# Performance work log

Hardware: AMD Instinct MI355X
Metric: run time of the kernel (lower is better)

## Reference

```python
import jax, jax.numpy as jnp
import numpy as np

N_NODES = 100000
D_FEAT = 128
UNITS = 128
N_EDGES = 600000


def setup_inputs() -> dict:
    key = jax.random.key(0)
    k1, k2, k3, k4, k5 = jax.random.split(key, 5)
    X = jax.random.normal(k1, (N_NODES, D_FEAT), dtype=jnp.float32)
    ref_a = jax.random.randint(k2, (N_EDGES,), 0, N_NODES, dtype=jnp.int32)
    ref_b = jax.random.randint(k3, (N_EDGES,), 0, N_NODES, dtype=jnp.int32)
    # Glorot-ish scaled dense weights
    W_hidden = jax.random.normal(k4, (D_FEAT, UNITS), dtype=jnp.float32) * (1.0 / np.sqrt(D_FEAT))
    W_out = jax.random.normal(k5, (UNITS, UNITS), dtype=jnp.float32) * (1.0 / np.sqrt(UNITS))
    b_hidden = jnp.zeros((UNITS,), dtype=jnp.float32)
    b_out = jnp.zeros((UNITS,), dtype=jnp.float32)
    return dict(X=X, ref_a=ref_a, ref_b=ref_b, W_hidden=W_hidden,
                b_hidden=b_hidden, W_out=W_out, b_out=b_out)


def wl1_convolution(X, ref_a, ref_b):
    # WL1 neighborhood aggregation over undirected edges (ref_a, ref_b):
    # each node keeps its own features plus the sum of its neighbors'.
    n = X.shape[0]
    agg_a = jax.ops.segment_sum(X[ref_b], ref_a, num_segments=n)  # [N, D]
    agg_b = jax.ops.segment_sum(X[ref_a], ref_b, num_segments=n)  # [N, D]
    return X + agg_a + agg_b


def reference(X, ref_a, ref_b, W_hidden, b_hidden, W_out, b_out):
    X_agg = wl1_convolution(X, ref_a, ref_b)                 # [N, D]
    X_hid = jax.nn.relu(X_agg @ W_hidden + b_hidden)          # [N, U] (inner_activation=relu)
    X_out = X_hid @ W_out + b_out                             # [N, U] (activation=linear)
    return X_out
```

## Files before the change

### kernel.cpp

```cpp
#include <hip/hip_runtime.h>

#define CAP 64

typedef short bf16x8 __attribute__((ext_vector_type(8)));
typedef float f32x4 __attribute__((ext_vector_type(4)));
typedef unsigned short u16;
typedef unsigned int u32;

__device__ __forceinline__ u16 f32_to_bf16(float f) {
  u32 b = __float_as_uint(f);
  b += 0x7fffu + ((b >> 16) & 1u);
  return (u16)(b >> 16);
}

__global__ void convert_x_kernel(const float* __restrict__ X,
                                 u16* __restrict__ Xb, int n8) {
  int i = blockIdx.x * blockDim.x + threadIdx.x;
  if (i >= n8) return;
  float4 a = ((const float4*)X)[2 * i];
  float4 b = ((const float4*)X)[2 * i + 1];
  int4 o;
  o.x = (int)((u32)f32_to_bf16(a.x) | ((u32)f32_to_bf16(a.y) << 16));
  o.y = (int)((u32)f32_to_bf16(a.z) | ((u32)f32_to_bf16(a.w) << 16));
  o.z = (int)((u32)f32_to_bf16(b.x) | ((u32)f32_to_bf16(b.y) << 16));
  o.w = (int)((u32)f32_to_bf16(b.z) | ((u32)f32_to_bf16(b.w) << 16));
  ((int4*)Xb)[i] = o;
}

__global__ __launch_bounds__(256) void fill_adj_xcd_kernel(
    const int* __restrict__ ra, const int* __restrict__ rb,
    int* __restrict__ cnt, int* __restrict__ adj, int nedges) {
  const int myx = blockIdx.x & 7;
  const int slice = blockIdx.x >> 3;
  int t = slice * 256 + threadIdx.x;
  int e0 = t * 2;
  if (e0 >= nedges) return;
  bool has1 = (e0 + 1) < nedges;
  int2 av = ((const int2*)ra)[t];
  int2 bv = ((const int2*)rb)[t];

  int d[4], s[4];
  d[0] = av.x; s[0] = bv.x;
  d[1] = bv.x; s[1] = av.x;
  d[2] = has1 ? av.y : -1; s[2] = bv.y;
  d[3] = has1 ? bv.y : -1; s[3] = av.y;
#pragma unroll
  for (int i = 0; i < 4; ++i) {
    if (d[i] >= 0 && (d[i] & 7) == myx) {
      int p = atomicAdd(&cnt[d[i]], 1);
      if (p < CAP) adj[(size_t)d[i] * CAP + p] = s[i];
    }
  }
}

__global__ void gather_agg_kernel(const u16* __restrict__ Xb,
                                  const int* __restrict__ cnt,
                                  int* __restrict__ adj,
                                  int nnodes) {
  int gid = blockIdx.x * blockDim.x + threadIdx.x;
  int wid = gid >> 6;
  int l = gid & 63;
  int half = l >> 5;
  int hl = l & 31;
  int node = wid * 2 + half;
  if (node >= nnodes) return;
  const uint2* Xv = (const uint2*)Xb;
  const int* lst = adj + (size_t)node * CAP;
  int idx0 = lst[hl];
  int idx1 = lst[hl + 32];
  int n = cnt[node];
  if (n > CAP) n = CAP;
  uint2 ps = Xv[(size_t)node * 32 + hl];
  float a0 = __uint_as_float(ps.x << 16);
  float a1 = __uint_as_float(ps.x & 0xffff0000u);
  float a2 = __uint_as_float(ps.y << 16);
  float a3 = __uint_as_float(ps.y & 0xffff0000u);
  const int base = half << 5;
  for (int k = 0; k < n; k += 8) {
    uint2 pv[8];
#pragma unroll
    for (int t = 0; t < 8; ++t) {
      int pos = k + t;
      int sel = (pos < 32) ? idx0 : idx1;
      int nb = __shfl(sel, base + (pos & 31));
      pv[t] = (pos < n) ? Xv[(size_t)nb * 32 + hl] : make_uint2(0u, 0u);
    }
#pragma unroll
    for (int t = 0; t < 8; ++t) {
      a0 += __uint_as_float(pv[t].x << 16);
      a1 += __uint_as_float(pv[t].x & 0xffff0000u);
      a2 += __uint_as_float(pv[t].y << 16);
      a3 += __uint_as_float(pv[t].y & 0xffff0000u);
    }
  }
  u32 w0 = (u32)f32_to_bf16(a0) | ((u32)f32_to_bf16(a1) << 16);
  u32 w1 = (u32)f32_to_bf16(a2) | ((u32)f32_to_bf16(a3) << 16);
  ((uint2*)adj)[(size_t)node * 32 + hl] = make_uint2(w0, w1);
}

__global__ void convert_w_kernel(const float* __restrict__ Wh,
                                 const float* __restrict__ Wo,
                                 u16* __restrict__ WhT,
                                 u16* __restrict__ WoT) {
  int idx = blockIdx.x * 256 + threadIdx.x;
  const float* src = (idx < 16384) ? Wh : Wo;
  u16* dst = (idx < 16384) ? WhT : WoT;
  int i = idx & 16383;
  int k = i >> 7, n = i & 127;
  dst[n * 128 + k] = f32_to_bf16(src[k * 128 + n]);
}

__global__ __launch_bounds__(256) void mlp_mfma_kernel(
    const u16* __restrict__ Xagg,
    const u16* __restrict__ WhT,
    const u16* __restrict__ WoT,
    const float* __restrict__ bh,
    const float* __restrict__ bo,
    float* __restrict__ out, int nnodes) {
  __shared__ u16 smem[2 * 128 * 128];
  u16* sA = smem;
  u16* sW = smem + 16384;

  const int tid = threadIdx.x;
  const int w = tid >> 6;
  const int l = tid & 63;
  const int l15 = l & 15;
  const int l4 = l >> 4;
  const int r0 = blockIdx.x * 128;

#pragma unroll
  for (int t = 0; t < 8; ++t) {
    int id = tid + t * 256;
    int r = id >> 4, u = id & 15;
    int gr = r0 + r;
    if (gr >= nnodes) gr = nnodes - 1;
    *(int4*)&sA[r * 128 + ((u ^ (r & 15)) * 8)] =
        *(const int4*)&Xagg[(size_t)gr * 128 + u * 8];
    *(int4*)&sW[r * 128 + ((u ^ (r & 15)) * 8)] =
        *(const int4*)&WhT[r * 128 + u * 8];
  }

  float bhv[8], bov[8];
#pragma unroll
  for (int j = 0; j < 8; ++j) {
    bhv[j] = bh[j * 16 + l15];
    bov[j] = bo[j * 16 + l15];
  }
  __syncthreads();

  const int m0 = w * 32 + l15;
  const int m1 = w * 32 + 16 + l15;

  f32x4 acc[2][8];
#pragma unroll
  for (int i = 0; i < 2; ++i)
#pragma unroll
    for (int j = 0; j < 8; ++j) acc[i][j] = (f32x4){0.f, 0.f, 0.f, 0.f};

#pragma unroll
  for (int c = 0; c < 4; ++c) {
    int pu = ((c * 4 + l4) ^ l15) * 8;
    bf16x8 a0 = *(bf16x8*)&sA[m0 * 128 + pu];
    bf16x8 a1 = *(bf16x8*)&sA[m1 * 128 + pu];
#pragma unroll
    for (int j = 0; j < 8; ++j) {
      bf16x8 bfr = *(bf16x8*)&sW[(j * 16 + l15) * 128 + pu];
      acc[0][j] = __builtin_amdgcn_mfma_f32_16x16x32_bf16(a0, bfr, acc[0][j], 0, 0, 0);
      acc[1][j] = __builtin_amdgcn_mfma_f32_16x16x32_bf16(a1, bfr, acc[1][j], 0, 0, 0);
    }
  }

  __syncthreads();

#pragma unroll
  for (int t = 0; t < 8; ++t) {
    int id = tid + t * 256;
    int r = id >> 4, u = id & 15;
    *(int4*)&sW[r * 128 + ((u ^ (r & 15)) * 8)] =
        *(const int4*)&WoT[r * 128 + u * 8];
  }

#pragma unroll
  for (int i = 0; i < 2; ++i)
#pragma unroll
    for (int j = 0; j < 8; ++j)
#pragma unroll
      for (int r = 0; r < 4; ++r) {
        int m = w * 32 + i * 16 + l4 * 4 + r;
        float v = fmaxf(acc[i][j][r] + bhv[j], 0.f);
        int k = j * 16 + l15;
        sA[m * 128 + (((k >> 3) ^ (m & 15)) * 8) + (k & 7)] = f32_to_bf16(v);
      }
  __syncthreads();

#pragma unroll
  for (int i = 0; i < 2; ++i)
#pragma unroll
    for (int j = 0; j < 8; ++j) acc[i][j] = (f32x4){0.f, 0.f, 0.f, 0.f};

#pragma unroll
  for (int c = 0; c < 4; ++c) {
    int pu = ((c * 4 + l4) ^ l15) * 8;
    bf16x8 a0 = *(bf16x8*)&sA[m0 * 128 + pu];
    bf16x8 a1 = *(bf16x8*)&sA[m1 * 128 + pu];
#pragma unroll
    for (int j = 0; j < 8; ++j) {
      bf16x8 bfr = *(bf16x8*)&sW[(j * 16 + l15) * 128 + pu];
      acc[0][j] = __builtin_amdgcn_mfma_f32_16x16x32_bf16(a0, bfr, acc[0][j], 0, 0, 0);
      acc[1][j] = __builtin_amdgcn_mfma_f32_16x16x32_bf16(a1, bfr, acc[1][j], 0, 0, 0);
    }
  }

  __syncthreads();

  float* sOut = (float*)smem;
#pragma unroll
  for (int i = 0; i < 2; ++i)
#pragma unroll
    for (int j = 0; j < 8; ++j)
#pragma unroll
      for (int r = 0; r < 4; ++r) {
        int m = w * 32 + i * 16 + l4 * 4 + r;
        sOut[m * 128 + j * 16 + l15] = acc[i][j][r] + bov[j];
      }
  __syncthreads();
#pragma unroll
  for (int t = 0; t < 16; ++t) {
    int id = tid + t * 256;
    int r = id >> 5, u4 = id & 31;
    int gr = r0 + r;
    if (gr < nnodes)
      ((float4*)out)[(size_t)gr * 32 + u4] = ((const float4*)sOut)[id];
  }
}

extern "C" void kernel_launch(void* const* d_in, const int* in_sizes, int n_in,
                              void* d_out, int out_size, void* d_ws,
                              size_t ws_size, hipStream_t stream) {
  const float* X = (const float*)d_in[0];
  const int* ra = (const int*)d_in[1];
  const int* rb = (const int*)d_in[2];
  const float* Wh = (const float*)d_in[3];
  const float* bh = (const float*)d_in[4];
  const float* Wo = (const float*)d_in[5];
  const float* bo = (const float*)d_in[6];
  float* out = (float*)d_out;

  int nnodes = in_sizes[0] / 128;
  int nedges = in_sizes[1];

  int* cnt = (int*)d_ws;
  int* adj = cnt + nnodes;
  u16* WhT = (u16*)d_ws;
  u16* WoT = WhT + 16384;
  u16* Xb = (u16*)d_out;

  int n8 = nnodes * 16;
  hipMemsetAsync(cnt, 0, (size_t)nnodes * 4, stream);
  convert_x_kernel<<<(n8 + 255) / 256, 256, 0, stream>>>(X, Xb, n8);
  int nslices = ((nedges + 1) / 2 + 255) / 256;
  fill_adj_xcd_kernel<<<nslices * 8, 256, 0, stream>>>(ra, rb, cnt, adj,
                                                       nedges);
  int nwaves = (nnodes + 1) / 2;
  gather_agg_kernel<<<(nwaves * 64 + 255) / 256, 256, 0, stream>>>(Xb, cnt,
                                                                   adj, nnodes);
  convert_w_kernel<<<128, 256, 0, stream>>>(Wh, Wo, WhT, WoT);
  mlp_mfma_kernel<<<(nnodes + 127) / 128, 256, 0, stream>>>(
      (const u16*)adj, WhT, WoT, bh, bo, out, nnodes);
}
```

Before: 231.3 us.

## Bucket adjacency lists by XCD so each XCD touches a contiguous region

Remaps the adjacency and count arrays so that nodes owned by the same XCD (node & 7) sit in one contiguous block (bucket = xcd*nx + node>>3). The intent is to keep atomic counters and adjacency writes from one XCD in a compact, L2-local region instead of interleaving across all XCDs. The gather and MLP kernels index through the same permutation. It also uses nontemporal loads for the edge arrays and skips loading the second half of the neighbor list when the count is at most 32. The gather and MLP kernels now read the permuted layout, which may scatter their row accesses.

```diff
diff --git a/kernel.cpp b/kernel.cpp
--- a/kernel.cpp
+++ b/kernel.cpp
@@ -29,15 +29,17 @@
 
 __global__ __launch_bounds__(256) void fill_adj_xcd_kernel(
     const int* __restrict__ ra, const int* __restrict__ rb,
-    int* __restrict__ cnt, int* __restrict__ adj, int nedges) {
+    int* __restrict__ cnt, int* __restrict__ adj, int nedges, int nx) {
   const int myx = blockIdx.x & 7;
   const int slice = blockIdx.x >> 3;
   int t = slice * 256 + threadIdx.x;
   int e0 = t * 2;
   if (e0 >= nedges) return;
   bool has1 = (e0 + 1) < nedges;
-  int2 av = ((const int2*)ra)[t];
-  int2 bv = ((const int2*)rb)[t];
+  long long apk = __builtin_nontemporal_load((const long long*)ra + t);
+  long long bpk = __builtin_nontemporal_load((const long long*)rb + t);
+  int2 av = make_int2((int)apk, (int)(apk >> 32));
+  int2 bv = make_int2((int)bpk, (int)(bpk >> 32));
 
   int d[4], s[4];
   d[0] = av.x; s[0] = bv.x;
@@ -47,8 +49,9 @@
 #pragma unroll
   for (int i = 0; i < 4; ++i) {
     if (d[i] >= 0 && (d[i] & 7) == myx) {
-      int p = atomicAdd(&cnt[d[i]], 1);
-      if (p < CAP) adj[(size_t)d[i] * CAP + p] = s[i];
+      int bkt = myx * nx + (d[i] >> 3);
+      int p = atomicAdd(&cnt[bkt], 1);
+      if (p < CAP) adj[(size_t)bkt * CAP + p] = s[i];
     }
   }
 }
@@ -56,7 +59,7 @@
 __global__ void gather_agg_kernel(const u16* __restrict__ Xb,
                                   const int* __restrict__ cnt,
                                   int* __restrict__ adj,
-                                  int nnodes) {
+                                  int nnodes, int nx) {
   int gid = blockIdx.x * blockDim.x + threadIdx.x;
   int wid = gid >> 6;
   int l = gid & 63;
@@ -65,11 +68,12 @@
   int node = wid * 2 + half;
   if (node >= nnodes) return;
   const uint2* Xv = (const uint2*)Xb;
-  const int* lst = adj + (size_t)node * CAP;
+  const int bkt = (node & 7) * nx + (node >> 3);
+  const int* lst = adj + (size_t)bkt * CAP;
+  int n = cnt[bkt];
+  if (n > CAP) n = CAP;
   int idx0 = lst[hl];
-  int idx1 = lst[hl + 32];
-  int n = cnt[node];
-  if (n > CAP) n = CAP;
+  int idx1 = (n > 32) ? lst[hl + 32] : 0;
   uint2 ps = Xv[(size_t)node * 32 + hl];
   float a0 = __uint_as_float(ps.x << 16);
   float a1 = __uint_as_float(ps.x & 0xffff0000u);
@@ -95,7 +99,7 @@
   }
   u32 w0 = (u32)f32_to_bf16(a0) | ((u32)f32_to_bf16(a1) << 16);
   u32 w1 = (u32)f32_to_bf16(a2) | ((u32)f32_to_bf16(a3) << 16);
-  ((uint2*)adj)[(size_t)node * 32 + hl] = make_uint2(w0, w1);
+  ((uint2*)adj)[(size_t)bkt * 32 + hl] = make_uint2(w0, w1);
 }
 
 __global__ void convert_w_kernel(const float* __restrict__ Wh,
@@ -116,7 +120,7 @@
     const u16* __restrict__ WoT,
     const float* __restrict__ bh,
     const float* __restrict__ bo,
-    float* __restrict__ out, int nnodes) {
+    float* __restrict__ out, int nnodes, int nx) {
   __shared__ u16 smem[2 * 128 * 128];
   u16* sA = smem;
   u16* sW = smem + 16384;
@@ -134,8 +138,9 @@
     int r = id >> 4, u = id & 15;
     int gr = r0 + r;
     if (gr >= nnodes) gr = nnodes - 1;
+    size_t xrow = (size_t)((gr & 7) * nx + (gr >> 3)) * 128;
     *(int4*)&sA[r * 128 + ((u ^ (r & 15)) * 8)] =
-        *(const int4*)&Xagg[(size_t)gr * 128 + u * 8];
+        *(const int4*)&Xagg[xrow + u * 8];
     *(int4*)&sW[r * 128 + ((u ^ (r & 15)) * 8)] =
         *(const int4*)&WhT[r * 128 + u * 8];
   }
@@ -248,23 +253,24 @@
 
   int nnodes = in_sizes[0] / 128;
   int nedges = in_sizes[1];
+  int nx = (nnodes + 7) / 8;
 
   int* cnt = (int*)d_ws;
-  int* adj = cnt + nnodes;
+  int* adj = cnt + (size_t)nx * 8;
   u16* WhT = (u16*)d_ws;
   u16* WoT = WhT + 16384;
   u16* Xb = (u16*)d_out;
 
   int n8 = nnodes * 16;
-  hipMemsetAsync(cnt, 0, (size_t)nnodes * 4, stream);
+  hipMemsetAsync(cnt, 0, (size_t)nx * 8 * 4, stream);
   convert_x_kernel<<<(n8 + 255) / 256, 256, 0, stream>>>(X, Xb, n8);
   int nslices = ((nedges + 1) / 2 + 255) / 256;
   fill_adj_xcd_kernel<<<nslices * 8, 256, 0, stream>>>(ra, rb, cnt, adj,
-                                                       nedges);
+                                                       nedges, nx);
   int nwaves = (nnodes + 1) / 2;
-  gather_agg_kernel<<<(nwaves * 64 + 255) / 256, 256, 0, stream>>>(Xb, cnt,
-                                                                   adj, nnodes);
+  gather_agg_kernel<<<(nwaves * 64 + 255) / 256, 256, 0, stream>>>(
+      Xb, cnt, adj, nnodes, nx);
   convert_w_kernel<<<128, 256, 0, stream>>>(Wh, Wo, WhT, WoT);
   mlp_mfma_kernel<<<(nnodes + 127) / 128, 256, 0, stream>>>(
-      (const u16*)adj, WhT, WoT, bh, bo, out, nnodes);
-}
+      (const u16*)adj, WhT, WoT, bh, bo, out, nnodes, nx);
+}
```

Measured after the change: 230.6 us. No clear change (-0.3%).

## Replace global-atomic adjacency fill with two-pass radix binning and fused X conversion

Applied to the files above, without the earlier changes.

Builds the per-node adjacency lists in two stages. First, edges are bucketed into bins of 256 nodes using shared-memory histograms, with one global atomic per bin per block. Second, a per-bin kernel uses LDS atomics to scatter neighbors into the fixed-capacity lists, which removes the per-edge global atomics and the 8x redundant XCD-partitioned edge passes. The X-to-bf16 conversion is fused into the same launch as the radix pass, and the gather skips loading the second index half when a node has few neighbors. The cost is an extra kernel and an intermediate binned buffer kept in the output scratch. Edges beyond the fixed bin capacity (4096) are silently dropped.

```diff
diff --git a/kernel.cpp b/kernel.cpp
--- a/kernel.cpp
+++ b/kernel.cpp
@@ -1,6 +1,8 @@
 #include <hip/hip_runtime.h>
 
 #define CAP 64
+#define BCAP 4096
+#define RADIX_UNITS 4096
 
 typedef short bf16x8 __attribute__((ext_vector_type(8)));
 typedef float f32x4 __attribute__((ext_vector_type(4)));
@@ -13,50 +15,100 @@
   return (u16)(b >> 16);
 }
 
-__global__ void convert_x_kernel(const float* __restrict__ X,
-                                 u16* __restrict__ Xb, int n8) {
-  int i = blockIdx.x * blockDim.x + threadIdx.x;
-  if (i >= n8) return;
-  float4 a = ((const float4*)X)[2 * i];
-  float4 b = ((const float4*)X)[2 * i + 1];
-  int4 o;
-  o.x = (int)((u32)f32_to_bf16(a.x) | ((u32)f32_to_bf16(a.y) << 16));
-  o.y = (int)((u32)f32_to_bf16(a.z) | ((u32)f32_to_bf16(a.w) << 16));
-  o.z = (int)((u32)f32_to_bf16(b.x) | ((u32)f32_to_bf16(b.y) << 16));
-  o.w = (int)((u32)f32_to_bf16(b.z) | ((u32)f32_to_bf16(b.w) << 16));
-  ((int4*)Xb)[i] = o;
-}
-
-__global__ __launch_bounds__(256) void fill_adj_xcd_kernel(
+__global__ __launch_bounds__(256) void front_kernel(
+    const float* __restrict__ X, u16* __restrict__ Xb, int n8,
     const int* __restrict__ ra, const int* __restrict__ rb,
-    int* __restrict__ cnt, int* __restrict__ adj, int nedges) {
-  const int myx = blockIdx.x & 7;
-  const int slice = blockIdx.x >> 3;
-  int t = slice * 256 + threadIdx.x;
-  int e0 = t * 2;
-  if (e0 >= nedges) return;
-  bool has1 = (e0 + 1) < nedges;
-  int2 av = ((const int2*)ra)[t];
-  int2 bv = ((const int2*)rb)[t];
-
-  int d[4], s[4];
-  d[0] = av.x; s[0] = bv.x;
-  d[1] = bv.x; s[1] = av.x;
-  d[2] = has1 ? av.y : -1; s[2] = bv.y;
-  d[3] = has1 ? bv.y : -1; s[3] = av.y;
-#pragma unroll
-  for (int i = 0; i < 4; ++i) {
-    if (d[i] >= 0 && (d[i] & 7) == myx) {
-      int p = atomicAdd(&cnt[d[i]], 1);
-      if (p < CAP) adj[(size_t)d[i] * CAP + p] = s[i];
-    }
-  }
+    int* __restrict__ gOff, int2* __restrict__ binned, int nedges, int nunits,
+    int nbins, int nradix) {
+  if ((int)blockIdx.x >= nradix) {
+    int i = ((int)blockIdx.x - nradix) * 256 + threadIdx.x;
+    if (i >= n8) return;
+    float4 a = ((const float4*)X)[2 * i];
+    float4 b = ((const float4*)X)[2 * i + 1];
+    int4 o;
+    o.x = (int)((u32)f32_to_bf16(a.x) | ((u32)f32_to_bf16(a.y) << 16));
+    o.y = (int)((u32)f32_to_bf16(a.z) | ((u32)f32_to_bf16(a.w) << 16));
+    o.z = (int)((u32)f32_to_bf16(b.x) | ((u32)f32_to_bf16(b.y) << 16));
+    o.w = (int)((u32)f32_to_bf16(b.z) | ((u32)f32_to_bf16(b.w) << 16));
+    ((int4*)Xb)[i] = o;
+    return;
+  }
+  __shared__ int lh[512];
+  const int tid = threadIdx.x;
+  for (int b = tid; b < nbins; b += 256) lh[b] = 0;
+  __syncthreads();
+  const int u0 = (int)blockIdx.x * RADIX_UNITS;
+
+  for (int k = 0; k < RADIX_UNITS / 256; ++k) {
+    int u = u0 + k * 256 + tid;
+    if (u < nunits) {
+      long long apk = ((const long long*)ra)[u];
+      long long bpk = ((const long long*)rb)[u];
+      int a0 = (int)apk, a1 = (int)(apk >> 32);
+      int b0 = (int)bpk, b1 = (int)(bpk >> 32);
+      bool has1 = (2 * u + 1) < nedges;
+      atomicAdd(&lh[a0 >> 8], 1);
+      atomicAdd(&lh[b0 >> 8], 1);
+      if (has1) {
+        atomicAdd(&lh[a1 >> 8], 1);
+        atomicAdd(&lh[b1 >> 8], 1);
+      }
+    }
+  }
+  __syncthreads();
+  for (int b = tid; b < nbins; b += 256) {
+    int c = lh[b];
+    lh[b] = (c > 0) ? atomicAdd(&gOff[b], c) : 0;
+  }
+  __syncthreads();
+  for (int k = 0; k < RADIX_UNITS / 256; ++k) {
+    int u = u0 + k * 256 + tid;
+    if (u < nunits) {
+      long long apk = ((const long long*)ra)[u];
+      long long bpk = ((const long long*)rb)[u];
+      int a0 = (int)apk, a1 = (int)(apk >> 32);
+      int b0 = (int)bpk, b1 = (int)(bpk >> 32);
+      bool has1 = (2 * u + 1) < nedges;
+      int d[4], s[4];
+      d[0] = a0; s[0] = b0;
+      d[1] = b0; s[1] = a0;
+      d[2] = has1 ? a1 : -1; s[2] = b1;
+      d[3] = has1 ? b1 : -1; s[3] = a1;
+#pragma unroll
+      for (int i = 0; i < 4; ++i) {
+        if (d[i] >= 0) {
+          int b = d[i] >> 8;
+          int slot = atomicAdd(&lh[b], 1);
+          if (slot < BCAP) binned[(size_t)b * BCAP + slot] = make_int2(d[i], s[i]);
+        }
+      }
+    }
+  }
+}
+
+__global__ __launch_bounds__(256) void bin_build_kernel(
+    const int2* __restrict__ binned, const int* __restrict__ gOff,
+    int* __restrict__ cnt, int* __restrict__ adj, int nnodes) {
+  __shared__ int lc[256];
+  const int bin = blockIdx.x;
+  lc[threadIdx.x] = 0;
+  __syncthreads();
+  int count = gOff[bin];
+  if (count > BCAP) count = BCAP;
+  const int2* src = binned + (size_t)bin * BCAP;
+  for (int i = threadIdx.x; i < count; i += 256) {
+    int2 e = src[i];
+    int p = atomicAdd(&lc[e.x & 255], 1);
+    if (p < CAP) adj[(size_t)e.x * CAP + p] = e.y;
+  }
+  __syncthreads();
+  int node = bin * 256 + threadIdx.x;
+  if (node < nnodes) cnt[node] = lc[threadIdx.x];
 }
 
 __global__ void gather_agg_kernel(const u16* __restrict__ Xb,
                                   const int* __restrict__ cnt,
-                                  int* __restrict__ adj,
-                                  int nnodes) {
+                                  int* __restrict__ adj, int nnodes) {
   int gid = blockIdx.x * blockDim.x + threadIdx.x;
   int wid = gid >> 6;
   int l = gid & 63;
@@ -66,10 +118,10 @@
   if (node >= nnodes) return;
   const uint2* Xv = (const uint2*)Xb;
   const int* lst = adj + (size_t)node * CAP;
-  int idx0 = lst[hl];
-  int idx1 = lst[hl + 32];
   int n = cnt[node];
   if (n > CAP) n = CAP;
+  int idx0 = lst[hl];
+  int idx1 = (n > 32) ? lst[hl + 32] : 0;
   uint2 ps = Xv[(size_t)node * 32 + hl];
   float a0 = __uint_as_float(ps.x << 16);
   float a1 = __uint_as_float(ps.x & 0xffff0000u);
@@ -248,19 +300,24 @@
 
   int nnodes = in_sizes[0] / 128;
   int nedges = in_sizes[1];
+  int nunits = (nedges + 1) / 2;
+  int nbins = (nnodes + 255) >> 8;
+  int nradix = (nunits + RADIX_UNITS - 1) / RADIX_UNITS;
 
   int* cnt = (int*)d_ws;
   int* adj = cnt + nnodes;
   u16* WhT = (u16*)d_ws;
   u16* WoT = WhT + 16384;
   u16* Xb = (u16*)d_out;
+  int2* binned = (int2*)((char*)d_out + (size_t)nnodes * 256);
+  int* gOff = (int*)((char*)binned + (size_t)nbins * BCAP * sizeof(int2));
 
   int n8 = nnodes * 16;
-  hipMemsetAsync(cnt, 0, (size_t)nnodes * 4, stream);
-  convert_x_kernel<<<(n8 + 255) / 256, 256, 0, stream>>>(X, Xb, n8);
-  int nslices = ((nedges + 1) / 2 + 255) / 256;
-  fill_adj_xcd_kernel<<<nslices * 8, 256, 0, stream>>>(ra, rb, cnt, adj,
-                                                       nedges);
+  int nconv = (n8 + 255) / 256;
+  hipMemsetAsync(gOff, 0, (size_t)nbins * 4, stream);
+  front_kernel<<<nradix + nconv, 256, 0, stream>>>(
+      X, Xb, n8, ra, rb, gOff, binned, nedges, nunits, nbins, nradix);
+  bin_build_kernel<<<nbins, 256, 0, stream>>>(binned, gOff, cnt, adj, nnodes);
   int nwaves = (nnodes + 1) / 2;
   gather_agg_kernel<<<(nwaves * 64 + 255) / 256, 256, 0, stream>>>(Xb, cnt,
                                                                    adj, nnodes);
```

New measurement: 211.6 us. 8.5% less time.
